# Kernel tuning notes

Hardware: AMD Instinct MI355X
Metric: run time of the kernel (lower is better)

## Reference

```python
import jax, jax.numpy as jnp
import numpy as np
from jax import lax

B, L, M, K = 4096, 1000, 16, 20
PRIOR_LOC, PRIOR_SCALE = -0.01, 0.001


def _motif_probs(x, w):
    # x: [B,4,L], w: [M,4*K] -> sigmoid(max_t conv(x, w_m)) : [B,M]
    kern = w.reshape(M, 4, K)
    scores = lax.conv_general_dilated(x, kern, (1,), 'VALID',
                                      dimension_numbers=('NCH', 'OIH', 'NCH'))  # [B,M,L-K+1]
    return jax.nn.sigmoid(scores.max(-1))


def _z(x, w):
    # pz_wyx_network: Bernoulli(p).log_prob(0) + log_prob(1) per motif, then softmax over motifs
    p = _motif_probs(x, w)                    # [B,M]
    lp = jnp.log(p) + jnp.log1p(-p)
    return jax.nn.softmax(lp, axis=-1)


def _kl(q_loc, q_scale):
    # KL(N(q_loc,q_scale) || N(PRIOR_LOC, PRIOR_SCALE)), summed over all dims
    return (jnp.log(PRIOR_SCALE / q_scale)
            + (q_scale ** 2 + (q_loc - PRIOR_LOC) ** 2) / (2.0 * PRIOR_SCALE ** 2)
            - 0.5).sum()


def setup_inputs() -> dict:
    key = jax.random.key(0)
    ks = jax.random.split(key, 6)
    x = jax.random.uniform(ks[0], (B, 4, L), dtype=jnp.float32)
    y = (jax.random.uniform(ks[1], (B,)) > 0.5).astype(jnp.float32)
    qw_loc = jax.random.normal(ks[2], (M, 4 * K), dtype=jnp.float32)
    qw_scale_raw = jax.random.normal(ks[3], (M, 4 * K), dtype=jnp.float32)
    gen_scale = jnp.full((1,), -15.0, dtype=jnp.float32)
    eps1 = jax.random.normal(ks[4], (M, 4 * K), dtype=jnp.float32)
    eps2 = jax.random.normal(ks[5], (M, 4 * K), dtype=jnp.float32)
    return dict(x=x, y=y, qw_loc=qw_loc, qw_scale_raw=qw_scale_raw,
                gen_scale=gen_scale, eps1=eps1, eps2=eps2)


def reference(x, y, qw_loc, qw_scale_raw, gen_scale, eps1, eps2):
    q_scale = jax.nn.softplus(qw_scale_raw)
    # --- ELBO assembly (forward) ---
    w1 = qw_loc + q_scale * eps1              # first rsample
    z = _z(x, w1)                             # [B,M]
    elbo = (z * jnp.log(1e-20 + z)).sum(1)    # [B]
    elbo = elbo + 2.0 * _kl(qw_loc, q_scale)  # KL added twice in original forward
    w2 = qw_loc + q_scale * eps2              # second rsample
    p = _motif_probs(x, w2)                   # [B,M] generative_loc per motif
    s = 1.0 / jax.nn.softplus(gen_scale)[0]
    eps = 1e-16
    gll = -jnp.log(eps + (eps + p) ** s + (eps + 1.0 - p) ** s)          # [B,M]
    # BCELoss() has reduction='mean' -> scalar per motif (log clamped at -100 like torch)
    bce = -(y[:, None] * jnp.clip(jnp.log(p), -100.0)
            + (1.0 - y)[:, None] * jnp.clip(jnp.log(1.0 - p), -100.0)).mean(0)  # [M]
    gll = gll - s * bce[None, :]
    elbo = elbo - (z * gll).sum(1)
    loss = elbo.mean()
    # --- predict: per-sample gathered kernel conv (batched via grouped conv) ---
    assign = _z(x, qw_loc).argmax(-1)         # [B] motif assignment per sample
    w_z = qw_loc[assign].reshape(B, 4, K)     # gathered per-sample kernels
    xg = x.reshape(1, B * 4, L)
    sc = lax.conv_general_dilated(xg, w_z, (1,), 'VALID',
                                  dimension_numbers=('NCH', 'OIH', 'NCH'),
                                  feature_group_count=B)                # [1,B,L-K+1]
    y_pred = jax.nn.sigmoid(sc[0].max(-1))    # [B]
    return loss, y_pred
```

## Files before the change

kernel.cpp:

```cpp
#include <hip/hip_runtime.h>
#include <math.h>

#define B_N 4096
#define TVALID 981

typedef _Float16 f16x8 __attribute__((ext_vector_type(8)));
typedef float f32x16 __attribute__((ext_vector_type(16)));
typedef unsigned int u32x2 __attribute__((ext_vector_type(2)));

#define WS_FRAG 0
#define WS_RED  3840

static __device__ __forceinline__ float softplus_f(float x) {
    return fmaxf(x, 0.f) + log1pf(expf(-fabsf(x)));
}
static __device__ __forceinline__ uint32_t pkh(_Float16 a, _Float16 b) {
    return (uint32_t)__builtin_bit_cast(unsigned short, a)
         | ((uint32_t)__builtin_bit_cast(unsigned short, b) << 16);
}
static __device__ __forceinline__ f16x8 mkfrag(u32x2 lo, u32x2 hi) {
    union { uint32_t u[4]; f16x8 v; } t;
    t.u[0] = lo.x; t.u[1] = lo.y; t.u[2] = hi.x; t.u[3] = hi.y;
    return t.v;
}
static __device__ __forceinline__ f16x8 mkbfrag(const uint32_t* q) {
    union { uint32_t u[4]; f16x8 v; } t;
    t.u[0] = q[0]; t.u[1] = q[1]; t.u[2] = q[2]; t.u[3] = q[3];
    return t.v;
}

__global__ void prep_kernel(const float* __restrict__ qw_loc,
                            const float* __restrict__ qw_scale_raw,
                            const float* __restrict__ gen_scale,
                            const float* __restrict__ eps1,
                            const float* __restrict__ eps2,
                            float* __restrict__ wsf) {
    int g = blockIdx.x * 256 + threadIdx.x;
    if (g == 960) {
        float* red = wsf + WS_RED;
        red[0] = 1.0f / softplus_f(gen_scale[0]);
        red[1] = 0.f;
        for (int i = 0; i < 32; ++i) red[2 + i] = 0.f;
    }
    if (g >= 960) return;
    const int lane = g & 63, set = g >> 6;
    const int grp = set / 5, s = set - grp * 5;
    const int h = lane >> 5, n = lane & 31, f = n & 15;
    const int var = (grp == 2) ? 2 : (n < 16 ? 0 : 1);
    const int spl = (grp == 2) ? (n < 16 ? 0 : 1) : grp;
    uint32_t d[4];
#pragma unroll
    for (int q = 0; q < 4; ++q) {
        unsigned short es[2];
#pragma unroll
        for (int e = 0; e < 2; ++e) {
            int j = 2 * q + e;
            int c = j & 3;
            int kk = 4 * s + 2 * h + (j >> 2);
            int idx = f * 80 + c * 20 + kk;
            float w = qw_loc[idx];
            if (var != 2) {
                float qs = softplus_f(qw_scale_raw[idx]);
                w += qs * (var == 0 ? eps1[idx] : eps2[idx]);
            }
            _Float16 h1 = (_Float16)w;
            _Float16 hv = spl ? (_Float16)(w - (float)h1) : h1;
            es[e] = __builtin_bit_cast(unsigned short, hv);
        }
        d[q] = (uint32_t)es[0] | ((uint32_t)es[1] << 16);
    }
    uint4* out4 = (uint4*)((uint32_t*)wsf + WS_FRAG);
    out4[set * 64 + lane] = make_uint4(d[0], d[1], d[2], d[3]);
}

__global__ __launch_bounds__(128, 3) void conv_kernel(const float* __restrict__ x,
                                                      const float* __restrict__ y,
                                                      const float* __restrict__ wsf,
                                                      float* __restrict__ red,
                                                      float* __restrict__ out) {
    __shared__ uint32_t xls[2][2048];
    __shared__ float maxs[2][48];

    const int tid = threadIdx.x, b = blockIdx.x;
    const int lane = tid & 63, wid = tid >> 6;

    uint32_t Bv[15][4];
    const uint4* fg = (const uint4*)((const uint32_t*)wsf + WS_FRAG);
#pragma unroll
    for (int u = 0; u < 15; ++u) {
        uint4 t = fg[u * 64 + lane];
        Bv[u][0] = t.x; Bv[u][1] = t.y; Bv[u][2] = t.z; Bv[u][3] = t.w;
    }

    const float* xb = x + (size_t)b * 4000;
#pragma unroll
    for (int j = 0; j < 4; ++j) {
        int p0 = 2 * (tid + 128 * j);
        float v[4][2];
        if (p0 < 1000) {
#pragma unroll
            for (int c = 0; c < 4; ++c) {
                float2 t = *(const float2*)(xb + c * 1000 + p0);
                v[c][0] = t.x; v[c][1] = t.y;
            }
        } else {
#pragma unroll
            for (int c = 0; c < 4; ++c) { v[c][0] = 0.f; v[c][1] = 0.f; }
        }
        uint32_t s0[4], s1[4];
#pragma unroll
        for (int e = 0; e < 2; ++e) {
            _Float16 a[4], r[4];
#pragma unroll
            for (int c = 0; c < 4; ++c) {
                a[c] = (_Float16)v[c][e];
                r[c] = (_Float16)(v[c][e] - (float)a[c]);
            }
            s0[2 * e + 0] = pkh(a[0], a[1]); s0[2 * e + 1] = pkh(a[2], a[3]);
            s1[2 * e + 0] = pkh(r[0], r[1]); s1[2 * e + 1] = pkh(r[2], r[3]);
        }
        *(uint4*)&xls[0][4 * (tid + 128 * j)] = make_uint4(s0[0], s0[1], s0[2], s0[3]);
        *(uint4*)&xls[1][4 * (tid + 128 * j)] = make_uint4(s1[0], s1[1], s1[2], s1[3]);
    }
    __syncthreads();

    const int i31 = lane & 31, h = lane >> 5;
    float vmW[16], vmL[16];
#pragma unroll
    for (int e = 0; e < 16; ++e) { vmW[e] = -INFINITY; vmL[e] = -INFINITY; }

    const int t_beg = wid ? 16 : 0, t_end = wid ? 31 : 16;
    for (int tile = t_beg; tile < t_end; ++tile) {
        const int tb = tile * 32;
        f32x16 accW, accL;
#pragma unroll
        for (int e = 0; e < 16; ++e) { accW[e] = 0.f; accL[e] = 0.f; }
#pragma unroll
        for (int s = 0; s < 5; ++s) {
            const int p = tb + i31 + 4 * s + 2 * h;
            u32x2 a0 = *(const u32x2*)&xls[0][2 * p];
            u32x2 a1 = *(const u32x2*)&xls[0][2 * p + 2];
            u32x2 b0 = *(const u32x2*)&xls[1][2 * p];
            u32x2 b1 = *(const u32x2*)&xls[1][2 * p + 2];
            f16x8 A1 = mkfrag(a0, a1);
            f16x8 A2 = mkfrag(b0, b1);
            f16x8 B0 = mkbfrag(Bv[s]);
            f16x8 B1 = mkbfrag(Bv[5 + s]);
            f16x8 B2 = mkbfrag(Bv[10 + s]);
            accW = __builtin_amdgcn_mfma_f32_32x32x16_f16(A1, B0, accW, 0, 0, 0);
            accL = __builtin_amdgcn_mfma_f32_32x32x16_f16(A1, B2, accL, 0, 0, 0);
            accW = __builtin_amdgcn_mfma_f32_32x32x16_f16(A1, B1, accW, 0, 0, 0);
            accL = __builtin_amdgcn_mfma_f32_32x32x16_f16(A2, B2, accL, 0, 0, 0);
            accW = __builtin_amdgcn_mfma_f32_32x32x16_f16(A2, B0, accW, 0, 0, 0);
        }
        if (tile < 30) {
#pragma unroll
            for (int e = 0; e < 16; ++e) {
                vmW[e] = fmaxf(vmW[e], accW[e]);
                float sum = accL[e] + __shfl_xor(accL[e], 16, 64);
                vmL[e] = fmaxf(vmL[e], sum);
            }
        } else {
#pragma unroll
            for (int e = 0; e < 16; ++e) {
                int row = (e & 3) + 8 * (e >> 2) + 4 * h;
                bool ok = (tb + row) < TVALID;
                vmW[e] = fmaxf(vmW[e], ok ? accW[e] : -INFINITY);
                float sum = accL[e] + __shfl_xor(accL[e], 16, 64);
                vmL[e] = fmaxf(vmL[e], ok ? sum : -INFINITY);
            }
        }
    }

    float mW = vmW[0], mL = vmL[0];
#pragma unroll
    for (int e = 1; e < 16; ++e) { mW = fmaxf(mW, vmW[e]); mL = fmaxf(mL, vmL[e]); }
    mW = fmaxf(mW, __shfl_xor(mW, 32, 64));
    mL = fmaxf(mL, __shfl_xor(mL, 32, 64));
    if (lane < 32) maxs[wid][lane] = mW;
    if (lane < 16) maxs[wid][32 + lane] = mL;
    __syncthreads();

    if (tid < 16) {
        const int m = tid;
        const float s_ = red[0];
        const float yb = y[b];
        float sc1 = fmaxf(maxs[0][m],      maxs[1][m]);
        float sc2 = fmaxf(maxs[0][16 + m], maxs[1][16 + m]);
        float sc0 = fmaxf(maxs[0][32 + m], maxs[1][32 + m]);

        float p1 = 1.f / (1.f + expf(-sc1));
        float lp = logf(p1) + log1pf(-p1);
        float mx = lp;
#pragma unroll
        for (int o = 8; o; o >>= 1) mx = fmaxf(mx, __shfl_xor(mx, o, 16));
        float e = expf(lp - mx);
        float se_ = e;
#pragma unroll
        for (int o = 8; o; o >>= 1) se_ += __shfl_xor(se_, o, 16);
        float z = e / se_;
        float Aterm = z * logf(1e-20f + z);

        float p2 = 1.f / (1.f + expf(-sc2));
        float g0 = -logf(1e-16f + powf(1e-16f + p2, s_) + powf(1.0f - p2, s_));
        float Cterm = z * g0;
        float bterm = yb * fmaxf(logf(p2), -100.f)
                    + (1.f - yb) * fmaxf(logf(1.f - p2), -100.f);

        float AC = Aterm - Cterm;
#pragma unroll
        for (int o = 8; o; o >>= 1) AC += __shfl_xor(AC, o, 16);

        atomicAdd(&red[2 + m], z);
        atomicAdd(&red[18 + m], bterm);

        float p0 = 1.f / (1.f + expf(-sc0));
        float lp0 = logf(p0) + log1pf(-p0);
        float best = lp0; int bidx = m;
#pragma unroll
        for (int o = 8; o; o >>= 1) {
            float ov = __shfl_xor(best, o, 16);
            int   oi = __shfl_xor(bidx, o, 16);
            if (ov > best || (ov == best && oi < bidx)) { best = ov; bidx = oi; }
        }
        if (m == 0) {
            atomicAdd(&red[1], AC);
            out[1 + b] = 1.f / (1.f + expf(-fmaxf(maxs[0][32 + bidx], maxs[1][32 + bidx])));
        }
    }
}

__global__ void finish_kernel(const float* __restrict__ qw_loc,
                              const float* __restrict__ qw_scale_raw,
                              const float* __restrict__ wsf,
                              float* __restrict__ out) {
    int tid = threadIdx.x;
    double kl = 0.0;
    for (int i = tid; i < 1280; i += 64) {
        float loc = qw_loc[i], qs = softplus_f(qw_scale_raw[i]);
        float dl = loc + 0.01f;
        kl += (double)(logf(0.001f / qs) + (qs * qs + dl * dl) / 2e-6f - 0.5f);
    }
#pragma unroll
    for (int o = 32; o; o >>= 1) kl += __shfl_xor(kl, o, 64);
    if (tid == 0) {
        const float* red = wsf + WS_RED;
        float t = 0.f;
        for (int m = 0; m < 16; ++m) t += red[2 + m] * red[18 + m];
        float loss = red[1] / 4096.0f + (float)(2.0 * kl)
                   - red[0] * (t / (4096.0f * 4096.0f));
        out[0] = loss;
    }
}

extern "C" void kernel_launch(void* const* d_in, const int* in_sizes, int n_in,
                              void* d_out, int out_size, void* d_ws, size_t ws_size,
                              hipStream_t stream) {
    const float* x            = (const float*)d_in[0];
    const float* y            = (const float*)d_in[1];
    const float* qw_loc       = (const float*)d_in[2];
    const float* qw_scale_raw = (const float*)d_in[3];
    const float* gen_scale    = (const float*)d_in[4];
    const float* eps1         = (const float*)d_in[5];
    const float* eps2         = (const float*)d_in[6];
    float* out = (float*)d_out;
    float* wsf = (float*)d_ws;

    prep_kernel<<<4, 256, 0, stream>>>(qw_loc, qw_scale_raw, gen_scale, eps1, eps2, wsf);
    conv_kernel<<<B_N, 128, 0, stream>>>(x, y, wsf, wsf + WS_RED, out);
    finish_kernel<<<1, 64, 0, stream>>>(qw_loc, qw_scale_raw, wsf, out);
}
```

Baseline: 282.8 us.

## Interleave hi/lo x halves in LDS, use 4 waves, drop accL shuffle

Stores the fp16 high and residual parts of x interleaved per position, so each MFMA A-fragment pair comes from two 16-byte LDS reads instead of four 8-byte reads. The loc-weight B fragments are reorganised into four groups, with a zero-padded lo group, so the unsampled-weight accumulator needs no cross-lane shuffle-add. That costs one extra MFMA per step. Block size doubles to 256 threads and the 31 tiles are spread across four waves, and the cross-wave max reduction is widened to match. The larger block raises register and LDS pressure per block and drops the explicit occupancy hint.

```diff
diff --git a/kernel.cpp b/kernel.cpp
--- a/kernel.cpp
+++ b/kernel.cpp
@@ -6,10 +6,9 @@
 
 typedef _Float16 f16x8 __attribute__((ext_vector_type(8)));
 typedef float f32x16 __attribute__((ext_vector_type(16)));
-typedef unsigned int u32x2 __attribute__((ext_vector_type(2)));
 
 #define WS_FRAG 0
-#define WS_RED  3840
+#define WS_RED  5120
 
 static __device__ __forceinline__ float softplus_f(float x) {
     return fmaxf(x, 0.f) + log1pf(expf(-fabsf(x)));
@@ -18,14 +17,9 @@
     return (uint32_t)__builtin_bit_cast(unsigned short, a)
          | ((uint32_t)__builtin_bit_cast(unsigned short, b) << 16);
 }
-static __device__ __forceinline__ f16x8 mkfrag(u32x2 lo, u32x2 hi) {
+static __device__ __forceinline__ f16x8 mkfrag(uint32_t d0, uint32_t d1, uint32_t d2, uint32_t d3) {
     union { uint32_t u[4]; f16x8 v; } t;
-    t.u[0] = lo.x; t.u[1] = lo.y; t.u[2] = hi.x; t.u[3] = hi.y;
-    return t.v;
-}
-static __device__ __forceinline__ f16x8 mkbfrag(const uint32_t* q) {
-    union { uint32_t u[4]; f16x8 v; } t;
-    t.u[0] = q[0]; t.u[1] = q[1]; t.u[2] = q[2]; t.u[3] = q[3];
+    t.u[0] = d0; t.u[1] = d1; t.u[2] = d2; t.u[3] = d3;
     return t.v;
 }
 
@@ -35,33 +29,35 @@
                             const float* __restrict__ eps1,
                             const float* __restrict__ eps2,
                             float* __restrict__ wsf) {
-    int g = blockIdx.x * 256 + threadIdx.x;
-    if (g == 960) {
-        float* red = wsf + WS_RED;
-        red[0] = 1.0f / softplus_f(gen_scale[0]);
-        red[1] = 0.f;
-        for (int i = 0; i < 32; ++i) red[2 + i] = 0.f;
-    }
-    if (g >= 960) return;
+    const int g = blockIdx.x * 256 + threadIdx.x;
+    float* red = wsf + WS_RED;
+    if (g == 0) red[0] = 1.0f / softplus_f(gen_scale[0]);
+    else if (g < 34) red[g] = 0.f;
+    if (g >= 1280) return;
+
     const int lane = g & 63, set = g >> 6;
     const int grp = set / 5, s = set - grp * 5;
     const int h = lane >> 5, n = lane & 31, f = n & 15;
-    const int var = (grp == 2) ? 2 : (n < 16 ? 0 : 1);
-    const int spl = (grp == 2) ? (n < 16 ? 0 : 1) : grp;
+    int var, spl;
+    if (grp == 0)      { var = (n < 16) ? 0 : 1; spl = 0; }
+    else if (grp == 1) { var = (n < 16) ? 0 : 1; spl = 1; }
+    else if (grp == 2) { var = 2;                spl = (n < 16) ? 0 : 1; }
+    else               { var = (n < 16) ? 2 : 3; spl = 1; }
+
     uint32_t d[4];
 #pragma unroll
     for (int q = 0; q < 4; ++q) {
         unsigned short es[2];
 #pragma unroll
         for (int e = 0; e < 2; ++e) {
-            int j = 2 * q + e;
-            int c = j & 3;
-            int kk = 4 * s + 2 * h + (j >> 2);
-            int idx = f * 80 + c * 20 + kk;
-            float w = qw_loc[idx];
-            if (var != 2) {
-                float qs = softplus_f(qw_scale_raw[idx]);
-                w += qs * (var == 0 ? eps1[idx] : eps2[idx]);
+            const int j = 2 * q + e;
+            const int c = j & 3;
+            const int kk = 4 * s + 2 * h + (j >> 2);
+            const int idx = f * 80 + c * 20 + kk;
+            float w = 0.f;
+            if (var != 3) {
+                w = qw_loc[idx];
+                if (var < 2) w += softplus_f(qw_scale_raw[idx]) * (var == 0 ? eps1[idx] : eps2[idx]);
             }
             _Float16 h1 = (_Float16)w;
             _Float16 hv = spl ? (_Float16)(w - (float)h1) : h1;
@@ -73,92 +69,90 @@
     out4[set * 64 + lane] = make_uint4(d[0], d[1], d[2], d[3]);
 }
 
-__global__ __launch_bounds__(128, 3) void conv_kernel(const float* __restrict__ x,
-                                                      const float* __restrict__ y,
-                                                      const float* __restrict__ wsf,
-                                                      float* __restrict__ red,
-                                                      float* __restrict__ out) {
-    __shared__ uint32_t xls[2][2048];
-    __shared__ float maxs[2][48];
+__global__ __launch_bounds__(256) void conv_kernel(const float* __restrict__ x,
+                                                   const float* __restrict__ y,
+                                                   const float* __restrict__ wsf,
+                                                   float* __restrict__ red,
+                                                   float* __restrict__ out) {
+    __shared__ __align__(16) uint32_t xls[4096];
+    __shared__ float maxs[4][48];
 
     const int tid = threadIdx.x, b = blockIdx.x;
     const int lane = tid & 63, wid = tid >> 6;
-
-    uint32_t Bv[15][4];
+    const int i31 = lane & 31, h = lane >> 5;
+
+    uint32_t Bv[20][4];
     const uint4* fg = (const uint4*)((const uint32_t*)wsf + WS_FRAG);
 #pragma unroll
-    for (int u = 0; u < 15; ++u) {
+    for (int u = 0; u < 20; ++u) {
         uint4 t = fg[u * 64 + lane];
         Bv[u][0] = t.x; Bv[u][1] = t.y; Bv[u][2] = t.z; Bv[u][3] = t.w;
     }
 
     const float* xb = x + (size_t)b * 4000;
 #pragma unroll
-    for (int j = 0; j < 4; ++j) {
-        int p0 = 2 * (tid + 128 * j);
-        float v[4][2];
-        if (p0 < 1000) {
+    for (int it = 0; it < 2; ++it) {
+        int u = tid + 256 * it;
+        if (u < 500) {
+            const int p0 = 2 * u;
+            float v[4][2];
 #pragma unroll
             for (int c = 0; c < 4; ++c) {
                 float2 t = *(const float2*)(xb + c * 1000 + p0);
                 v[c][0] = t.x; v[c][1] = t.y;
             }
-        } else {
-#pragma unroll
-            for (int c = 0; c < 4; ++c) { v[c][0] = 0.f; v[c][1] = 0.f; }
-        }
-        uint32_t s0[4], s1[4];
-#pragma unroll
-        for (int e = 0; e < 2; ++e) {
-            _Float16 a[4], r[4];
-#pragma unroll
-            for (int c = 0; c < 4; ++c) {
-                a[c] = (_Float16)v[c][e];
-                r[c] = (_Float16)(v[c][e] - (float)a[c]);
-            }
-            s0[2 * e + 0] = pkh(a[0], a[1]); s0[2 * e + 1] = pkh(a[2], a[3]);
-            s1[2 * e + 0] = pkh(r[0], r[1]); s1[2 * e + 1] = pkh(r[2], r[3]);
-        }
-        *(uint4*)&xls[0][4 * (tid + 128 * j)] = make_uint4(s0[0], s0[1], s0[2], s0[3]);
-        *(uint4*)&xls[1][4 * (tid + 128 * j)] = make_uint4(s1[0], s1[1], s1[2], s1[3]);
-    }
+#pragma unroll
+            for (int e = 0; e < 2; ++e) {
+                _Float16 a[4], r[4];
+#pragma unroll
+                for (int c = 0; c < 4; ++c) {
+                    a[c] = (_Float16)v[c][e];
+                    r[c] = (_Float16)(v[c][e] - (float)a[c]);
+                }
+                *(uint4*)&xls[4 * (p0 + e)] =
+                    make_uint4(pkh(a[0], a[1]), pkh(a[2], a[3]),
+                               pkh(r[0], r[1]), pkh(r[2], r[3]));
+            }
+        }
+    }
+    if (tid < 24) *(uint4*)&xls[4 * (1000 + tid)] = make_uint4(0, 0, 0, 0);
     __syncthreads();
 
-    const int i31 = lane & 31, h = lane >> 5;
     float vmW[16], vmL[16];
 #pragma unroll
     for (int e = 0; e < 16; ++e) { vmW[e] = -INFINITY; vmL[e] = -INFINITY; }
 
-    const int t_beg = wid ? 16 : 0, t_end = wid ? 31 : 16;
+    const int t_beg = wid * 8;
+    const int t_end = (wid == 3) ? 31 : (t_beg + 8);
     for (int tile = t_beg; tile < t_end; ++tile) {
         const int tb = tile * 32;
         f32x16 accW, accL;
 #pragma unroll
         for (int e = 0; e < 16; ++e) { accW[e] = 0.f; accL[e] = 0.f; }
+        const int Pb = tb + i31 + 2 * h;
 #pragma unroll
         for (int s = 0; s < 5; ++s) {
-            const int p = tb + i31 + 4 * s + 2 * h;
-            u32x2 a0 = *(const u32x2*)&xls[0][2 * p];
-            u32x2 a1 = *(const u32x2*)&xls[0][2 * p + 2];
-            u32x2 b0 = *(const u32x2*)&xls[1][2 * p];
-            u32x2 b1 = *(const u32x2*)&xls[1][2 * p + 2];
-            f16x8 A1 = mkfrag(a0, a1);
-            f16x8 A2 = mkfrag(b0, b1);
-            f16x8 B0 = mkbfrag(Bv[s]);
-            f16x8 B1 = mkbfrag(Bv[5 + s]);
-            f16x8 B2 = mkbfrag(Bv[10 + s]);
-            accW = __builtin_amdgcn_mfma_f32_32x32x16_f16(A1, B0, accW, 0, 0, 0);
-            accL = __builtin_amdgcn_mfma_f32_32x32x16_f16(A1, B2, accL, 0, 0, 0);
-            accW = __builtin_amdgcn_mfma_f32_32x32x16_f16(A1, B1, accW, 0, 0, 0);
-            accL = __builtin_amdgcn_mfma_f32_32x32x16_f16(A2, B2, accL, 0, 0, 0);
-            accW = __builtin_amdgcn_mfma_f32_32x32x16_f16(A2, B0, accW, 0, 0, 0);
+            const int P = Pb + 4 * s;
+            uint4 q0 = *(const uint4*)&xls[4 * P];
+            uint4 q1 = *(const uint4*)&xls[4 * P + 4];
+            f16x8 A1 = mkfrag(q0.x, q0.y, q1.x, q1.y);
+            f16x8 A2 = mkfrag(q0.z, q0.w, q1.z, q1.w);
+            f16x8 B0  = mkfrag(Bv[s][0],      Bv[s][1],      Bv[s][2],      Bv[s][3]);
+            f16x8 B1  = mkfrag(Bv[5+s][0],    Bv[5+s][1],    Bv[5+s][2],    Bv[5+s][3]);
+            f16x8 B2a = mkfrag(Bv[10+s][0],   Bv[10+s][1],   Bv[10+s][2],   Bv[10+s][3]);
+            f16x8 B2b = mkfrag(Bv[15+s][0],   Bv[15+s][1],   Bv[15+s][2],   Bv[15+s][3]);
+            accW = __builtin_amdgcn_mfma_f32_32x32x16_f16(A1, B0,  accW, 0, 0, 0);
+            accL = __builtin_amdgcn_mfma_f32_32x32x16_f16(A1, B2a, accL, 0, 0, 0);
+            accW = __builtin_amdgcn_mfma_f32_32x32x16_f16(A1, B1,  accW, 0, 0, 0);
+            accL = __builtin_amdgcn_mfma_f32_32x32x16_f16(A1, B2b, accL, 0, 0, 0);
+            accW = __builtin_amdgcn_mfma_f32_32x32x16_f16(A2, B0,  accW, 0, 0, 0);
+            accL = __builtin_amdgcn_mfma_f32_32x32x16_f16(A2, B2a, accL, 0, 0, 0);
         }
         if (tile < 30) {
 #pragma unroll
             for (int e = 0; e < 16; ++e) {
                 vmW[e] = fmaxf(vmW[e], accW[e]);
-                float sum = accL[e] + __shfl_xor(accL[e], 16, 64);
-                vmL[e] = fmaxf(vmL[e], sum);
+                vmL[e] = fmaxf(vmL[e], accL[e]);
             }
         } else {
 #pragma unroll
@@ -166,8 +160,7 @@
                 int row = (e & 3) + 8 * (e >> 2) + 4 * h;
                 bool ok = (tb + row) < TVALID;
                 vmW[e] = fmaxf(vmW[e], ok ? accW[e] : -INFINITY);
-                float sum = accL[e] + __shfl_xor(accL[e], 16, 64);
-                vmL[e] = fmaxf(vmL[e], ok ? sum : -INFINITY);
+                vmL[e] = fmaxf(vmL[e], ok ? accL[e] : -INFINITY);
             }
         }
     }
@@ -185,9 +178,12 @@
         const int m = tid;
         const float s_ = red[0];
         const float yb = y[b];
-        float sc1 = fmaxf(maxs[0][m],      maxs[1][m]);
-        float sc2 = fmaxf(maxs[0][16 + m], maxs[1][16 + m]);
-        float sc0 = fmaxf(maxs[0][32 + m], maxs[1][32 + m]);
+        float sc1 = fmaxf(fmaxf(maxs[0][m],      maxs[1][m]),
+                          fmaxf(maxs[2][m],      maxs[3][m]));
+        float sc2 = fmaxf(fmaxf(maxs[0][16 + m], maxs[1][16 + m]),
+                          fmaxf(maxs[2][16 + m], maxs[3][16 + m]));
+        float sc0 = fmaxf(fmaxf(maxs[0][32 + m], maxs[1][32 + m]),
+                          fmaxf(maxs[2][32 + m], maxs[3][32 + m]));
 
         float p1 = 1.f / (1.f + expf(-sc1));
         float lp = logf(p1) + log1pf(-p1);
@@ -225,7 +221,9 @@
         }
         if (m == 0) {
             atomicAdd(&red[1], AC);
-            out[1 + b] = 1.f / (1.f + expf(-fmaxf(maxs[0][32 + bidx], maxs[1][32 + bidx])));
+            float scb = fmaxf(fmaxf(maxs[0][32 + bidx], maxs[1][32 + bidx]),
+                              fmaxf(maxs[2][32 + bidx], maxs[3][32 + bidx]));
+            out[1 + b] = 1.f / (1.f + expf(-scb));
         }
     }
 }
@@ -266,7 +264,7 @@
     float* out = (float*)d_out;
     float* wsf = (float*)d_ws;
 
-    prep_kernel<<<4, 256, 0, stream>>>(qw_loc, qw_scale_raw, gen_scale, eps1, eps2, wsf);
-    conv_kernel<<<B_N, 128, 0, stream>>>(x, y, wsf, wsf + WS_RED, out);
+    prep_kernel<<<5, 256, 0, stream>>>(qw_loc, qw_scale_raw, gen_scale, eps1, eps2, wsf);
+    conv_kernel<<<B_N, 256, 0, stream>>>(x, y, wsf, wsf + WS_RED, out);
     finish_kernel<<<1, 64, 0, stream>>>(qw_loc, qw_scale_raw, wsf, out);
 }
```

Measured after the change: 270.3 us. -4.4%, faster.
